# Kernel tuning notes

Hardware: AMD Instinct MI355X
Metric: run time of the kernel (lower is better)

## Reference

```python
import jax, jax.numpy as jnp
import numpy as np

N_HEADS = 16
N_KV_HEADS = 8
DIM = 2048
HEAD_DIM = DIM // N_HEADS  # 128
N_REP = N_HEADS // N_KV_HEADS


def _rope(t, cos, sin):
    # t: [B, S, H, D]; cos/sin: [S, D//2]
    t2 = t.reshape(*t.shape[:-1], -1, 2)  # [B,S,H,D/2,2]
    p1, p2 = t2[..., 0], t2[..., 1]
    c = cos[None, :, None, :]
    s = sin[None, :, None, :]
    r1 = p1 * c - p2 * s
    r2 = p1 * s + p2 * c
    return jnp.stack((r1, r2), axis=-1).reshape(t.shape)


def setup_inputs() -> dict:
    key = jax.random.key(0)
    ks = jax.random.split(key, 7)
    B, S = 2, 2048
    x = jax.random.normal(ks[0], (B, S, DIM), dtype=jnp.float32)
    freqs_cos = jax.random.normal(ks[1], (S, HEAD_DIM // 2), dtype=jnp.float32)
    freqs_sin = jax.random.normal(ks[2], (S, HEAD_DIM // 2), dtype=jnp.float32)
    sc = 1.0 / np.sqrt(DIM)
    wq = jax.random.normal(ks[3], (DIM, N_HEADS * HEAD_DIM), dtype=jnp.float32) * sc
    wk = jax.random.normal(ks[4], (DIM, N_KV_HEADS * HEAD_DIM), dtype=jnp.float32) * sc
    wv = jax.random.normal(ks[5], (DIM, N_KV_HEADS * HEAD_DIM), dtype=jnp.float32) * sc
    wo = jax.random.normal(ks[6], (N_HEADS * HEAD_DIM, DIM), dtype=jnp.float32) * sc
    return {"x": x, "freqs_cos": freqs_cos, "freqs_sin": freqs_sin,
            "wq": wq, "wk": wk, "wv": wv, "wo": wo}


def reference(x, freqs_cos, freqs_sin, wq, wk, wv, wo):
    B, S, _ = x.shape
    xq = (x @ wq).reshape(B, S, N_HEADS, HEAD_DIM)
    xk = (x @ wk).reshape(B, S, N_KV_HEADS, HEAD_DIM)
    xv = (x @ wv).reshape(B, S, N_KV_HEADS, HEAD_DIM)
    xq = _rope(xq, freqs_cos, freqs_sin)
    xk = _rope(xk, freqs_cos, freqs_sin)
    # GQA repeat_kv: [B,S,Hkv,D] -> [B,S,Hkv*n_rep,D]
    xk = jnp.repeat(xk, N_REP, axis=2)
    xv = jnp.repeat(xv, N_REP, axis=2)
    q = xq.transpose(0, 2, 1, 3)  # [B,H,S,D]
    k = xk.transpose(0, 2, 1, 3)
    v = xv.transpose(0, 2, 1, 3)
    scale = 1.0 / np.sqrt(HEAD_DIM)
    scores = jnp.einsum('bhqd,bhkd->bhqk', q, k) * scale
    causal = jnp.tril(jnp.ones((S, S), dtype=bool))
    scores = jnp.where(causal[None, None], scores, -jnp.inf)
    probs = jax.nn.softmax(scores.astype(jnp.float32), axis=-1).astype(q.dtype)
    out = jnp.einsum('bhqk,bhkd->bhqd', probs, v)
    out = out.transpose(0, 2, 1, 3).reshape(B, S, N_HEADS * HEAD_DIM)
    return out @ wo
```

## Files before the change

### kernel.cpp

```cpp
#include <hip/hip_runtime.h>
#include <cstdint>
#include <cstddef>

#define S_LEN 2048
#define DIM_   2048
#define NH   16
#define NKV  8
#define HD   128

typedef __attribute__((ext_vector_type(8))) __bf16 bf16x8;
typedef __attribute__((ext_vector_type(4))) float  f32x4;

typedef const __attribute__((address_space(1))) void* gptr_t;
typedef __attribute__((address_space(3))) void*       sptr_t;

static __device__ __forceinline__ float bf2f(unsigned short u) {
  union { unsigned int i; float f; } v; v.i = ((unsigned int)u) << 16; return v.f;
}
static __device__ __forceinline__ unsigned short f2bf(float f) {
  union { float f; unsigned int i; } v; v.f = f;
  unsigned int u = v.i;
  unsigned int r = (u + 0x7FFFu + ((u >> 16) & 1u)) >> 16;
  return (unsigned short)r;
}
static __device__ __forceinline__ unsigned int cvt_pk_bf16(float a, float b) {
  unsigned int r;
  asm volatile("v_cvt_pk_bf16_f32 %0, %1, %2" : "=v"(r) : "v"(a), "v"(b));
  return r;
}

#define QSCALE 0.12751744f
#define RESC_THR 11.542f

__global__ void k_prep(const float* __restrict__ x, unsigned short* __restrict__ xb,
                       const float* __restrict__ wq, const float* __restrict__ wk,
                       const float* __restrict__ wv, const float* __restrict__ wo,
                       unsigned short* __restrict__ wqkvT, unsigned short* __restrict__ woT) {
  int bid = blockIdx.x;
  if (bid < 8192) {
    int i = bid * 256 + threadIdx.x;
    float4 v = ((const float4*)x)[i];
    ushort4 o; o.x = f2bf(v.x); o.y = f2bf(v.y); o.z = f2bf(v.z); o.w = f2bf(v.w);
    ((ushort4*)xb)[i] = o;
    return;
  }
  bid -= 8192;
  const float* src; unsigned short* dst; int N, ntx;
  if (bid < 1024)      { src = wq; dst = wqkvT;                       N = 2048; ntx = 32; }
  else if (bid < 1536) { bid -= 1024; src = wk; dst = wqkvT + (size_t)2048 * 2048; N = 1024; ntx = 16; }
  else if (bid < 2048) { bid -= 1536; src = wv; dst = wqkvT + (size_t)3072 * 2048; N = 1024; ntx = 16; }
  else                 { bid -= 2048; src = wo; dst = woT;            N = 2048; ntx = 32; }
  const int K = 2048;
  __shared__ float tile[64][65];
  int lx = threadIdx.x & 15, ly = threadIdx.x >> 4;
  int r0 = (bid / ntx) * 64, c0 = (bid % ntx) * 64;
  #pragma unroll
  for (int i = 0; i < 4; i++) {
    int row = ly + 16 * i;
    float4 v = *(const float4*)(&src[(size_t)(r0 + row) * N + c0 + lx * 4]);
    tile[row][lx * 4 + 0] = v.x; tile[row][lx * 4 + 1] = v.y;
    tile[row][lx * 4 + 2] = v.z; tile[row][lx * 4 + 3] = v.w;
  }
  __syncthreads();
  #pragma unroll
  for (int i = 0; i < 4; i++) {
    int nrow = ly + 16 * i;
    ushort4 o;
    o.x = f2bf(tile[lx * 4 + 0][nrow]); o.y = f2bf(tile[lx * 4 + 1][nrow]);
    o.z = f2bf(tile[lx * 4 + 2][nrow]); o.w = f2bf(tile[lx * 4 + 3][nrow]);
    *(ushort4*)(&dst[(size_t)(c0 + nrow) * K + r0 + lx * 4]) = o;
  }
}

template<int MODE, int BM_, int TPB>
__global__ __launch_bounds__(TPB, 2) void k_gemm_bt(
    const unsigned short* __restrict__ A, const unsigned short* __restrict__ BT,
    void* __restrict__ C, int N, int K,
    const float* __restrict__ fc, const float* __restrict__ fs,
    unsigned short* __restrict__ kb, unsigned short* __restrict__ vb) {
  constexpr int NI = (BM_ == 64) ? 2 : 4;
  constexpr int AR = (BM_ * 64) / (TPB * 8);
  constexpr int BR = (128 * 64) / (TPB * 8);
  __shared__ __align__(16) unsigned short Asm[BM_ * 64];
  __shared__ __align__(16) unsigned short Bsm[128 * 64];
  const int t = threadIdx.x;
  const int lane = t & 63, w = t >> 6;
  const int wm = (BM_ == 64) ? 0 : (w >> 1) * 64;
  const int wn = (BM_ == 64) ? w * 32 : (w & 1) * 64;
  const int col = lane & 15, quad = lane >> 4;
  const int m0 = blockIdx.y * BM_, n0 = blockIdx.x * 128;

  f32x4 acc[4][NI];
  #pragma unroll
  for (int i = 0; i < 4; i++)
    #pragma unroll
    for (int j = 0; j < NI; j++) acc[i][j] = (f32x4){0.f, 0.f, 0.f, 0.f};

  for (int kk = 0; kk < K; kk += 64) {
    #pragma unroll
    for (int r = 0; r < AR; ++r) {
      int c = t + r * TPB;
      int c0 = (t & ~63) + r * TPB;
      int row = c >> 3;
      int kcs = (c & 7) ^ (row & 7);
      const unsigned short* gA = A + (size_t)(m0 + row) * K + kk + kcs * 8;
      __builtin_amdgcn_global_load_lds((gptr_t)gA, (sptr_t)(&Asm[c0 * 8]), 16, 0, 0);
    }
    #pragma unroll
    for (int r = 0; r < BR; ++r) {
      int c = t + r * TPB;
      int c0 = (t & ~63) + r * TPB;
      int row = c >> 3;
      int kcs = (c & 7) ^ (row & 7);
      const unsigned short* gB = BT + (size_t)(n0 + row) * K + kk + kcs * 8;
      __builtin_amdgcn_global_load_lds((gptr_t)gB, (sptr_t)(&Bsm[c0 * 8]), 16, 0, 0);
    }
    __syncthreads();
    #pragma unroll
    for (int kc2 = 0; kc2 < 2; kc2++) {
      bf16x8 af[4], bf[NI];
      #pragma unroll
      for (int mi = 0; mi < 4; mi++) {
        int rowA = wm + mi * 16 + col;
        af[mi] = *(const bf16x8*)(&Asm[rowA * 64 + (((kc2 * 4 + quad) ^ (col & 7)) * 8)]);
      }
      #pragma unroll
      for (int ni = 0; ni < NI; ni++) {
        int rowB = wn + ni * 16 + col;
        bf[ni] = *(const bf16x8*)(&Bsm[rowB * 64 + (((kc2 * 4 + quad) ^ (col & 7)) * 8)]);
      }
      #pragma unroll
      for (int mi = 0; mi < 4; mi++)
        #pragma unroll
        for (int ni = 0; ni < NI; ni++)
          acc[mi][ni] = __builtin_amdgcn_mfma_f32_16x16x32_bf16(af[mi], bf[ni], acc[mi][ni], 0, 0, 0);
    }
    __syncthreads();
  }

  #pragma unroll
  for (int mi = 0; mi < 4; mi++) {
    int row_base = m0 + wm + mi * 16 + quad * 4;
    #pragma unroll
    for (int ni = 0; ni < NI; ni++) {
      int col_g = n0 + wn + ni * 16 + col;
      if (MODE == 1) {
        float* O = (float*)C;
        #pragma unroll
        for (int r = 0; r < 4; r++) O[(size_t)(row_base + r) * N + col_g] = acc[mi][ni][r];
      } else {
        int region = col_g >> 10;
        if (region < 3) {
          int ri = (col_g & 127) >> 1;
          float sgn = (col_g & 1) ? 1.f : -1.f;
          unsigned short* qO = (unsigned short*)C;
          #pragma unroll
          for (int r = 0; r < 4; r++) {
            int row = row_base + r;
            int s = row & (S_LEN - 1);
            float cv = fc[s * 64 + ri], sv = fs[s * 64 + ri];
            float val = acc[mi][ni][r];
            float other = __shfl_xor(val, 1);
            float res = val * cv + sgn * other * sv;
            if (region < 2) qO[(size_t)row * 2048 + col_g] = f2bf(res * QSCALE);
            else            kb[(size_t)row * 1024 + (col_g - 2048)] = f2bf(res);
          }
        } else {
          int n_local = col_g - 3072;
          int b = row_base >> 11, s = row_base & (S_LEN - 1);
          int kvh = n_local >> 7, d = n_local & (HD - 1);
          ushort4 o4;
          o4.x = f2bf(acc[mi][ni][0]); o4.y = f2bf(acc[mi][ni][1]);
          o4.z = f2bf(acc[mi][ni][2]); o4.w = f2bf(acc[mi][ni][3]);
          *(ushort4*)(&vb[((size_t)((b * NKV + kvh) * HD + d)) * S_LEN + s]) = o4;
        }
      }
    }
  }
}

#define KLD 136
#define VLD 72
#define PLD 72
__global__ __launch_bounds__(256, 3) void k_attn(
    const unsigned short* __restrict__ q, const unsigned short* __restrict__ k,
    const unsigned short* __restrict__ vT, unsigned short* __restrict__ ao) {
  __shared__ __align__(16) unsigned short Ksm[64 * KLD];
  __shared__ __align__(16) unsigned short Vsm[128 * VLD];
  __shared__ __align__(16) unsigned short Psm[4 * 16 * PLD];
  const int t = threadIdx.x;
  const int lane = t & 63, w = t >> 6;
  const int col = lane & 15, quad = lane >> 4;
  const int bh = blockIdx.x;
  const int b = bh >> 4, h = bh & 15;
  const int kvh = h >> 1;
  const int my_qt = 31 - blockIdx.y;
  const int qrow = my_qt * 64 + w * 16;
  unsigned short* Pw = &Psm[w * 16 * PLD];

  const int ki = t >> 4, kdc = t & 15;
  const int vd = t >> 3, vkc = t & 7;
  const unsigned short* kg = k + ((size_t)(b * S_LEN + ki)) * (NKV * HD) + kvh * HD + kdc * 8;
  const unsigned short* vg = vT + ((size_t)((b * NKV + kvh) * HD + vd)) * S_LEN + vkc * 8;
  const size_t KROW = (size_t)16 * (NKV * HD);
  const size_t VROW = (size_t)32 * S_LEN;
  const size_t KSTEP = (size_t)64 * (NKV * HD);
  const size_t VSTEP = 64;

  bf16x8 qf[4];
  const size_t qbase = ((size_t)(b * S_LEN) + qrow + col) * DIM_ + h * HD;
  #pragma unroll
  for (int kc = 0; kc < 4; kc++) qf[kc] = *(const bf16x8*)(q + qbase + kc * 32 + quad * 8);

  f32x4 o[8];
  #pragma unroll
  for (int i = 0; i < 8; i++) o[i] = (f32x4){0.f, 0.f, 0.f, 0.f};
  float m_i = -1e30f;
  float l_i = 0.f;

  const int nkt = my_qt + 1;

  {
    #pragma unroll
    for (int cc = 0; cc < 4; cc++) {
      uint4 kr = *(const uint4*)(kg + cc * KROW);
      *(uint4*)(&Ksm[(ki + cc * 16) * KLD + kdc * 8]) = kr;
      uint4 vr = *(const uint4*)(vg + cc * VROW);
      *(uint4*)(&Vsm[(vd + cc * 32) * VLD + vkc * 8]) = vr;
    }
  }
  __syncthreads();

  for (int kt = 0; kt < nkt; ++kt) {
    const bool more = (kt + 1 < nkt);
    uint4 kr0, kr1, kr2, kr3, vr0, vr1, vr2, vr3;
    if (more) {
      kg += KSTEP; vg += VSTEP;
      kr0 = *(const uint4*)(kg + 0 * KROW);
      kr1 = *(const uint4*)(kg + 1 * KROW);
      kr2 = *(const uint4*)(kg + 2 * KROW);
      kr3 = *(const uint4*)(kg + 3 * KROW);
      vr0 = *(const uint4*)(vg + 0 * VROW);
      vr1 = *(const uint4*)(vg + 1 * VROW);
      vr2 = *(const uint4*)(vg + 2 * VROW);
      vr3 = *(const uint4*)(vg + 3 * VROW);
    }

    float p[4][4];
    __builtin_amdgcn_s_setprio(1);
    #pragma unroll
    for (int nt = 0; nt < 4; nt++) {
      f32x4 s_acc = (f32x4){0.f, 0.f, 0.f, 0.f};
      #pragma unroll
      for (int kc = 0; kc < 4; kc++) {
        bf16x8 kf = *(const bf16x8*)(&Ksm[(nt * 16 + col) * KLD + kc * 32 + quad * 8]);
        s_acc = __builtin_amdgcn_mfma_f32_16x16x32_bf16(kf, qf[kc], s_acc, 0, 0, 0);
      }
      #pragma unroll
      for (int r = 0; r < 4; r++) p[nt][r] = s_acc[r];
    }
    __builtin_amdgcn_s_setprio(0);

    if (kt == my_qt) {
      const int qglob = qrow + col;
      #pragma unroll
      for (int nt = 0; nt < 4; nt++)
        #pragma unroll
        for (int r = 0; r < 4; r++)
          if (kt * 64 + nt * 16 + quad * 4 + r > qglob) p[nt][r] = -1e30f;
    }

    float mx = fmaxf(fmaxf(fmaxf(p[0][0], p[0][1]), fmaxf(p[0][2], p[0][3])),
                     fmaxf(fmaxf(p[1][0], p[1][1]), fmaxf(p[1][2], p[1][3])));
    mx = fmaxf(mx, fmaxf(fmaxf(fmaxf(p[2][0], p[2][1]), fmaxf(p[2][2], p[2][3])),
                         fmaxf(fmaxf(p[3][0], p[3][1]), fmaxf(p[3][2], p[3][3]))));
    float mxs = fmaxf(mx, __shfl_xor(mx, 16));
    mxs = fmaxf(mxs, __shfl_xor(mxs, 32));
    float pe[4][4];
    #pragma unroll
    for (int nt = 0; nt < 4; nt++)
      #pragma unroll
      for (int r = 0; r < 4; r++) pe[nt][r] = exp2f(p[nt][r] - m_i);
    float rs = ((pe[0][0] + pe[0][1]) + (pe[0][2] + pe[0][3]))
             + ((pe[1][0] + pe[1][1]) + (pe[1][2] + pe[1][3]))
             + ((pe[2][0] + pe[2][1]) + (pe[2][2] + pe[2][3]))
             + ((pe[3][0] + pe[3][1]) + (pe[3][2] + pe[3][3]));
    if (__any(mxs - m_i > RESC_THR)) {
      float mn = fmaxf(m_i, mxs);
      float alpha = exp2f(m_i - mn);
      m_i = mn; l_i *= alpha;
      float ar[4];
      #pragma unroll
      for (int r = 0; r < 4; r++) ar[r] = __shfl(alpha, quad * 4 + r);
      #pragma unroll
      for (int dt = 0; dt < 8; dt++)
        #pragma unroll
        for (int r = 0; r < 4; r++) o[dt][r] *= ar[r];
      #pragma unroll
      for (int nt = 0; nt < 4; nt++)
        #pragma unroll
        for (int r = 0; r < 4; r++) pe[nt][r] = exp2f(p[nt][r] - m_i);
      rs = ((pe[0][0] + pe[0][1]) + (pe[0][2] + pe[0][3]))
         + ((pe[1][0] + pe[1][1]) + (pe[1][2] + pe[1][3]))
         + ((pe[2][0] + pe[2][1]) + (pe[2][2] + pe[2][3]))
         + ((pe[3][0] + pe[3][1]) + (pe[3][2] + pe[3][3]));
    }
    rs += __shfl_xor(rs, 16);
    rs += __shfl_xor(rs, 32);
    l_i += rs;

    #pragma unroll
    for (int nt = 0; nt < 4; nt++) {
      uint2 pk;
      pk.x = cvt_pk_bf16(pe[nt][0], pe[nt][1]);
      pk.y = cvt_pk_bf16(pe[nt][2], pe[nt][3]);
      *(uint2*)(&Pw[col * PLD + nt * 16 + quad * 4]) = pk;
    }

    __syncthreads();

    if (more) {
      *(uint4*)(&Ksm[(ki +  0) * KLD + kdc * 8]) = kr0;
      *(uint4*)(&Ksm[(ki + 16) * KLD + kdc * 8]) = kr1;
      *(uint4*)(&Ksm[(ki + 32) * KLD + kdc * 8]) = kr2;
      *(uint4*)(&Ksm[(ki + 48) * KLD + kdc * 8]) = kr3;
    }

    bf16x8 pf[2];
    #pragma unroll
    for (int kc2 = 0; kc2 < 2; kc2++)
      pf[kc2] = *(const bf16x8*)(&Pw[col * PLD + kc2 * 32 + quad * 8]);

    __builtin_amdgcn_s_setprio(1);
    #pragma unroll
    for (int dt = 0; dt < 8; dt++) {
      #pragma unroll
      for (int kc2 = 0; kc2 < 2; kc2++) {
        bf16x8 vf = *(const bf16x8*)(&Vsm[(dt * 16 + col) * VLD + kc2 * 32 + quad * 8]);
        o[dt] = __builtin_amdgcn_mfma_f32_16x16x32_bf16(pf[kc2], vf, o[dt], 0, 0, 0);
      }
    }
    __builtin_amdgcn_s_setprio(0);

    __syncthreads();

    if (more) {
      *(uint4*)(&Vsm[(vd +  0) * VLD + vkc * 8]) = vr0;
      *(uint4*)(&Vsm[(vd + 32) * VLD + vkc * 8]) = vr1;
      *(uint4*)(&Vsm[(vd + 64) * VLD + vkc * 8]) = vr2;
      *(uint4*)(&Vsm[(vd + 96) * VLD + vkc * 8]) = vr3;
    }
  }

  float linv[4];
  #pragma unroll
  for (int r = 0; r < 4; r++) linv[r] = 1.f / __shfl(l_i, quad * 4 + r);
  #pragma unroll
  for (int dt = 0; dt < 8; dt++) {
    int dcol = h * HD + dt * 16 + col;
    #pragma unroll
    for (int r = 0; r < 4; r++) {
      int rg = qrow + quad * 4 + r;
      ao[((size_t)(b * S_LEN) + rg) * DIM_ + dcol] = f2bf(o[dt][r] * linv[r]);
    }
  }
}

extern "C" void kernel_launch(void* const* d_in, const int* in_sizes, int n_in,
                              void* d_out, int out_size, void* d_ws, size_t ws_size,
                              hipStream_t stream) {
  const float* x  = (const float*)d_in[0];
  const float* fc = (const float*)d_in[1];
  const float* fs = (const float*)d_in[2];
  const float* wq = (const float*)d_in[3];
  const float* wk = (const float*)d_in[4];
  const float* wv = (const float*)d_in[5];
  const float* wo = (const float*)d_in[6];
  float* out = (float*)d_out;

  char* ws = (char*)d_ws;
  const size_t MB = 1024 * 1024;
  unsigned short* xb    = (unsigned short*)(ws + 0 * MB);
  unsigned short* wqkvT = (unsigned short*)(ws + 16 * MB);
  unsigned short* woT   = (unsigned short*)(ws + 32 * MB);
  unsigned short* qb    = (unsigned short*)(ws + 40 * MB);
  unsigned short* kb    = (unsigned short*)(ws + 56 * MB);
  unsigned short* vT    = (unsigned short*)(ws + 64 * MB);
  unsigned short* ao    = (unsigned short*)(ws + 72 * MB);

  k_prep<<<dim3(11264), dim3(256), 0, stream>>>(x, xb, wq, wk, wv, wo, wqkvT, woT);
  k_gemm_bt<3, 128, 256><<<dim3(32, 32), dim3(256), 0, stream>>>(xb, wqkvT, (void*)qb, 4096, 2048, fc, fs, kb, vT);
  k_attn<<<dim3(32, 32), dim3(256), 0, stream>>>(qb, kb, vT, ao);
  k_gemm_bt<1, 64, 256><<<dim3(16, 64), dim3(256), 0, stream>>>(ao, woT, (void*)out, 2048, 2048, nullptr, nullptr, nullptr, nullptr);
}
```

Before: 334.4 us.

## Double-buffer K/V tiles in LDS and drop mid-loop barrier

The attention kernel now keeps two LDS buffers each for the K and V tiles. Prefetched tiles are written into the idle buffer after the PV MFMAs, so each loop iteration needs one block-wide barrier instead of two. A per-wave lgkmcnt wait replaces the barrier that guarded the per-wave P tile. The cost is roughly double the LDS per block, so the launch bound drops from 3 to 2 blocks per CU and there are fewer waves to hide latency.

```diff
diff --git a/kernel.cpp b/kernel.cpp
--- a/kernel.cpp
+++ b/kernel.cpp
@@ -182,11 +182,11 @@
 #define KLD 136
 #define VLD 72
 #define PLD 72
-__global__ __launch_bounds__(256, 3) void k_attn(
+__global__ __launch_bounds__(256, 2) void k_attn(
     const unsigned short* __restrict__ q, const unsigned short* __restrict__ k,
     const unsigned short* __restrict__ vT, unsigned short* __restrict__ ao) {
-  __shared__ __align__(16) unsigned short Ksm[64 * KLD];
-  __shared__ __align__(16) unsigned short Vsm[128 * VLD];
+  __shared__ __align__(16) unsigned short Ksm[2][64 * KLD];
+  __shared__ __align__(16) unsigned short Vsm[2][128 * VLD];
   __shared__ __align__(16) unsigned short Psm[4 * 16 * PLD];
   const int t = threadIdx.x;
   const int lane = t & 63, w = t >> 6;
@@ -224,14 +224,15 @@
     #pragma unroll
     for (int cc = 0; cc < 4; cc++) {
       uint4 kr = *(const uint4*)(kg + cc * KROW);
-      *(uint4*)(&Ksm[(ki + cc * 16) * KLD + kdc * 8]) = kr;
+      *(uint4*)(&Ksm[0][(ki + cc * 16) * KLD + kdc * 8]) = kr;
       uint4 vr = *(const uint4*)(vg + cc * VROW);
-      *(uint4*)(&Vsm[(vd + cc * 32) * VLD + vkc * 8]) = vr;
+      *(uint4*)(&Vsm[0][(vd + cc * 32) * VLD + vkc * 8]) = vr;
     }
   }
   __syncthreads();
 
   for (int kt = 0; kt < nkt; ++kt) {
+    const int cur = kt & 1, nxt = cur ^ 1;
     const bool more = (kt + 1 < nkt);
     uint4 kr0, kr1, kr2, kr3, vr0, vr1, vr2, vr3;
     if (more) {
@@ -253,7 +254,7 @@
       f32x4 s_acc = (f32x4){0.f, 0.f, 0.f, 0.f};
       #pragma unroll
       for (int kc = 0; kc < 4; kc++) {
-        bf16x8 kf = *(const bf16x8*)(&Ksm[(nt * 16 + col) * KLD + kc * 32 + quad * 8]);
+        bf16x8 kf = *(const bf16x8*)(&Ksm[cur][(nt * 16 + col) * KLD + kc * 32 + quad * 8]);
         s_acc = __builtin_amdgcn_mfma_f32_16x16x32_bf16(kf, qf[kc], s_acc, 0, 0, 0);
       }
       #pragma unroll
@@ -316,16 +317,7 @@
       pk.y = cvt_pk_bf16(pe[nt][2], pe[nt][3]);
       *(uint2*)(&Pw[col * PLD + nt * 16 + quad * 4]) = pk;
     }
-
-    __syncthreads();
-
-    if (more) {
-      *(uint4*)(&Ksm[(ki +  0) * KLD + kdc * 8]) = kr0;
-      *(uint4*)(&Ksm[(ki + 16) * KLD + kdc * 8]) = kr1;
-      *(uint4*)(&Ksm[(ki + 32) * KLD + kdc * 8]) = kr2;
-      *(uint4*)(&Ksm[(ki + 48) * KLD + kdc * 8]) = kr3;
-    }
-
+    asm volatile("s_waitcnt lgkmcnt(0)" ::: "memory");
     bf16x8 pf[2];
     #pragma unroll
     for (int kc2 = 0; kc2 < 2; kc2++)
@@ -336,20 +328,24 @@
     for (int dt = 0; dt < 8; dt++) {
       #pragma unroll
       for (int kc2 = 0; kc2 < 2; kc2++) {
-        bf16x8 vf = *(const bf16x8*)(&Vsm[(dt * 16 + col) * VLD + kc2 * 32 + quad * 8]);
+        bf16x8 vf = *(const bf16x8*)(&Vsm[cur][(dt * 16 + col) * VLD + kc2 * 32 + quad * 8]);
         o[dt] = __builtin_amdgcn_mfma_f32_16x16x32_bf16(pf[kc2], vf, o[dt], 0, 0, 0);
       }
     }
     __builtin_amdgcn_s_setprio(0);
 
+    if (more) {
+      *(uint4*)(&Ksm[nxt][(ki +  0) * KLD + kdc * 8]) = kr0;
+      *(uint4*)(&Ksm[nxt][(ki + 16) * KLD + kdc * 8]) = kr1;
+      *(uint4*)(&Ksm[nxt][(ki + 32) * KLD + kdc * 8]) = kr2;
+      *(uint4*)(&Ksm[nxt][(ki + 48) * KLD + kdc * 8]) = kr3;
+      *(uint4*)(&Vsm[nxt][(vd +  0) * VLD + vkc * 8]) = vr0;
+      *(uint4*)(&Vsm[nxt][(vd + 32) * VLD + vkc * 8]) = vr1;
+      *(uint4*)(&Vsm[nxt][(vd + 64) * VLD + vkc * 8]) = vr2;
+      *(uint4*)(&Vsm[nxt][(vd + 96) * VLD + vkc * 8]) = vr3;
+    }
+
     __syncthreads();
-
-    if (more) {
-      *(uint4*)(&Vsm[(vd +  0) * VLD + vkc * 8]) = vr0;
-      *(uint4*)(&Vsm[(vd + 32) * VLD + vkc * 8]) = vr1;
-      *(uint4*)(&Vsm[(vd + 64) * VLD + vkc * 8]) = vr2;
-      *(uint4*)(&Vsm[(vd + 96) * VLD + vkc * 8]) = vr3;
-    }
   }
 
   float linv[4];
```

Result: no change. 338.3 us (+1.2%).
